# Optimization experiments

Hardware: AMD Instinct MI355X
Metric: run time of the kernel (lower is better)

## Reference

```python
import jax, jax.numpy as jnp
import numpy as np

# Faithful distillation of AttentionNet's cross-modal attention block.
# The resnet50/PointNet backbones are replaced by their output feature maps
# (img: [B,256,64,64], pc2d: [B,2048,64,64]) supplied as inputs, since the
# kernel-relevant math is the conv1x1 projections + bmm/softmax/bmm attention,
# followed by global avg-pool, concat, and the fc + log_softmax head.
# Note: the original forward contains a bug (img_v1 overwritten by img.view)
# and dead code; we implement the clearly intended attention math.

B, CQ, CK, H, W = 16, 256, 2048, 64, 64
NUM_CLASS = 40


def conv1x1(x, w, b):
    # x: [B,Cin,H,W], w: [Cout,Cin], b: [Cout]
    return jnp.einsum('bchw,oc->bohw', x, w) + b[None, :, None, None]


def setup_inputs() -> dict:
    key = jax.random.key(0)
    ks = jax.random.split(key, 16)
    s = lambda fan_in: 1.0 / np.sqrt(fan_in)
    return {
        'img': jax.random.normal(ks[0], (B, CQ, H, W), jnp.float32),
        'pc2d': jax.random.normal(ks[1], (B, CK, H, W), jnp.float32),
        'Wq': jax.random.normal(ks[2], (CQ, CQ), jnp.float32) * s(CQ),
        'bq': jnp.zeros((CQ,), jnp.float32),
        'Wk': jax.random.normal(ks[3], (CQ, CK), jnp.float32) * s(CK),
        'bk': jnp.zeros((CQ,), jnp.float32),
        'Wvi': jax.random.normal(ks[4], (CQ, CQ), jnp.float32) * s(CQ),
        'bvi': jnp.zeros((CQ,), jnp.float32),
        'Wvp': jax.random.normal(ks[5], (CK, CK), jnp.float32) * s(CK),
        'bvp': jnp.zeros((CK,), jnp.float32),
        'gamma1': jnp.zeros((1,), jnp.float32),
        'W1': jax.random.normal(ks[6], (1024, CQ + CK), jnp.float32) * s(CQ + CK),
        'b1': jnp.zeros((1024,), jnp.float32),
        'W2': jax.random.normal(ks[7], (NUM_CLASS, 1024), jnp.float32) * s(1024),
        'b2': jnp.zeros((NUM_CLASS,), jnp.float32),
    }


def reference(img, pc2d, Wq, bq, Wk, bk, Wvi, bvi, Wvp, bvp, gamma1, W1, b1, W2, b2):
    N = H * W  # 4096
    q = conv1x1(img, Wq, bq).reshape(B, CQ, N).transpose(0, 2, 1)   # [B,N,256]
    k = conv1x1(pc2d, Wk, bk).reshape(B, CQ, N)                     # [B,256,N]
    att = jax.nn.softmax(jnp.einsum('bnc,bcm->bnm', q, k), axis=-1)  # [B,N,N]
    # image branch: out = gamma * bmm(V_img, att^T) + img
    vi = conv1x1(img, Wvi, bvi).reshape(B, CQ, N)
    img_att = jnp.einsum('bcn,bmn->bcm', vi, att).reshape(B, CQ, H, W)
    img_out = gamma1[0] * img_att + img
    # point-cloud branch: bmm(V_pc, att^T)
    vp = conv1x1(pc2d, Wvp, bvp).reshape(B, CK, N)
    pc_out = jnp.einsum('bcn,bmn->bcm', vp, att)                    # [B,2048,N]
    # global average pool + concat + MLP head with log_softmax
    img_feat = img_out.mean(axis=(2, 3))                            # [B,256]
    pc_feat = pc_out.mean(axis=2)                                   # [B,2048]
    fused = jnp.concatenate([img_feat, pc_feat], axis=-1)           # [B,2304]
    h = jax.nn.relu(fused @ W1.T + b1)
    logits = h @ W2.T + b2
    return jax.nn.log_softmax(logits, axis=1)
```

## Files before the change

### kernel.cpp

```cpp
#include <hip/hip_runtime.h>
#include <cstdint>

typedef __attribute__((ext_vector_type(8))) short short8;
typedef __attribute__((ext_vector_type(4))) float f32x4;

#define LOG2E 1.44269504088896340736f
#define SHIFT 64.0f

__device__ __forceinline__ unsigned short f2bf(float x) {
  union { float f; unsigned u; } c; c.f = x;
  unsigned r = c.u + 0x7fffu + ((c.u >> 16) & 1u);
  return (unsigned short)(r >> 16);
}

__device__ __forceinline__ void gl2lds16(const void* g, void* l) {
  __builtin_amdgcn_global_load_lds((const __attribute__((address_space(1))) void*)g,
                                   (__attribute__((address_space(3))) void*)l, 16, 0, 0);
}

__global__ void cvt_bf16(const float* __restrict__ src, unsigned short* __restrict__ dst, int n4) {
  int i = blockIdx.x * 256 + threadIdx.x;
  if (i >= n4) return;
  float4 v = ((const float4*)src)[i];
  ushort4 o;
  o.x = f2bf(v.x); o.y = f2bf(v.y); o.z = f2bf(v.z); o.w = f2bf(v.w);
  ((ushort4*)dst)[i] = o;
}

__device__ __forceinline__ void stage_tile_async(unsigned short* lds, const unsigned short* src,
                                                 int w, int lane) {
  const int r8 = lane >> 3;
  const int gx = (lane & 7) ^ r8;
  const char* gbase = (const char*)src + (size_t)(w * 32 + r8) * 512 + gx * 16;
  char* lbase = (char*)lds + (w * 32) * 128;
#pragma unroll
  for (int p = 0; p < 4; ++p)
    gl2lds16(gbase + (size_t)p * 8 * 512, lbase + p * 1024);
}

__device__ __forceinline__ void mfma_step(const unsigned short* A, const unsigned short* B,
                                          int aBase, int bBase, const int poff0, const int poff1,
                                          f32x4 acc[4][4]) {
#pragma unroll
  for (int ks = 0; ks < 2; ++ks) {
    const int po = ks ? poff1 : poff0;
    short8 af[4], bfr[4];
#pragma unroll
    for (int mt = 0; mt < 4; ++mt) af[mt] = *(const short8*)&A[aBase + mt * 1024 + po];
#pragma unroll
    for (int nt = 0; nt < 4; ++nt) bfr[nt] = *(const short8*)&B[bBase + nt * 1024 + po];
#pragma unroll
    for (int mt = 0; mt < 4; ++mt)
#pragma unroll
      for (int nt = 0; nt < 4; ++nt)
        acc[mt][nt] = __builtin_amdgcn_mfma_f32_16x16x32_bf16(af[mt], bfr[nt], acc[mt][nt], 0, 0, 0);
  }
}

__global__ __launch_bounds__(256, 2) void attn_rowsum(
    const unsigned short* __restrict__ qt, const unsigned short* __restrict__ kt,
    float* __restrict__ row_l) {
  __shared__ unsigned short Ab[2][128 * 64];
  __shared__ unsigned short Bb[2][128 * 64];
  __shared__ float lred[2][128];
  const int b = blockIdx.y, i0 = blockIdx.x * 128;
  const int t = threadIdx.x, w = t >> 6, lane = t & 63, q = lane >> 4, ln = lane & 15;
  const int ihalf = w >> 1, jhalf = w & 1;
  const unsigned short* qbase = qt + ((size_t)b * 4096 + i0) * 256;
  const unsigned short* kbase = kt + (size_t)b * 4096 * 256;
  const int poff0 = ((q) ^ (ln & 7)) * 8;
  const int poff1 = ((4 + q) ^ (ln & 7)) * 8;
  const int aBase = (ihalf * 64 + ln) * 64;
  const int bBase = (jhalf * 64 + ln) * 64;
  float lacc[4][4] = {};

  stage_tile_async(Ab[0], qbase, w, lane);
  stage_tile_async(Bb[0], kbase, w, lane);
  __syncthreads();

  for (int jt = 0; jt < 32; ++jt) {
    f32x4 acc[4][4] = {};
#pragma unroll 1
    for (int ch = 0; ch < 4; ++ch) {
      const int s = jt * 4 + ch;
      if (s + 1 < 128) {
        const int jn = (s + 1) >> 2, cn = (s + 1) & 3;
        stage_tile_async(Ab[(s + 1) & 1], qbase + cn * 64, w, lane);
        stage_tile_async(Bb[(s + 1) & 1], kbase + (size_t)jn * 128 * 256 + cn * 64, w, lane);
      }
      mfma_step(Ab[s & 1], Bb[s & 1], aBase, bBase, poff0, poff1, acc);
      __syncthreads();
    }
#pragma unroll
    for (int mt = 0; mt < 4; ++mt)
#pragma unroll
      for (int r = 0; r < 4; ++r) {
        float e = exp2f(acc[mt][0][r] * LOG2E - SHIFT) + exp2f(acc[mt][1][r] * LOG2E - SHIFT)
                + exp2f(acc[mt][2][r] * LOG2E - SHIFT) + exp2f(acc[mt][3][r] * LOG2E - SHIFT);
        e += __shfl_xor(e, 1); e += __shfl_xor(e, 2);
        e += __shfl_xor(e, 4); e += __shfl_xor(e, 8);
        lacc[mt][r] += e;
      }
  }
  if (ln == 0) {
#pragma unroll
    for (int mt = 0; mt < 4; ++mt)
#pragma unroll
      for (int r = 0; r < 4; ++r)
        lred[jhalf][ihalf * 64 + mt * 16 + q * 4 + r] = lacc[mt][r];
  }
  __syncthreads();
  if (t < 128) row_l[b * 4096 + i0 + t] = lred[0][t] + lred[1][t];
}

__global__ void inv_kernel(const float* __restrict__ l, float* __restrict__ linv) {
  int i = blockIdx.x * 256 + threadIdx.x;
  linv[i] = 1.0f / l[i];
}

__global__ __launch_bounds__(256, 2) void attn_colsum(
    const unsigned short* __restrict__ qt, const unsigned short* __restrict__ kt,
    const float* __restrict__ linv, float* __restrict__ s_col) {
  __shared__ unsigned short Ab[2][128 * 64];
  __shared__ unsigned short Bb[2][128 * 64];
  __shared__ float sred[2][128];
  const int b = blockIdx.y, j0 = blockIdx.x * 128;
  const int t = threadIdx.x, w = t >> 6, lane = t & 63, q = lane >> 4, ln = lane & 15;
  const int ihalf = w >> 1, jhalf = w & 1;
  const unsigned short* qbase = qt + (size_t)b * 4096 * 256;
  const unsigned short* kb = kt + ((size_t)b * 4096 + j0) * 256;
  const int poff0 = ((q) ^ (ln & 7)) * 8;
  const int poff1 = ((4 + q) ^ (ln & 7)) * 8;
  const int aBase = (ihalf * 64 + ln) * 64;
  const int bBase = (jhalf * 64 + ln) * 64;
  float scacc[4] = {};

  stage_tile_async(Ab[0], qbase, w, lane);
  stage_tile_async(Bb[0], kb, w, lane);
  __syncthreads();

  for (int it = 0; it < 32; ++it) {
    const float4* lp = (const float4*)(linv + (size_t)b * 4096 + it * 128 + ihalf * 64 + q * 4);
    float4 lv[4];
#pragma unroll
    for (int mt = 0; mt < 4; ++mt) lv[mt] = lp[mt * 4];

    f32x4 acc[4][4] = {};
#pragma unroll 1
    for (int ch = 0; ch < 4; ++ch) {
      const int s = it * 4 + ch;
      if (s + 1 < 128) {
        const int in_ = (s + 1) >> 2, cn = (s + 1) & 3;
        stage_tile_async(Ab[(s + 1) & 1], qbase + (size_t)in_ * 128 * 256 + cn * 64, w, lane);
        stage_tile_async(Bb[(s + 1) & 1], kb + cn * 64, w, lane);
      }
      mfma_step(Ab[s & 1], Bb[s & 1], aBase, bBase, poff0, poff1, acc);
      __syncthreads();
    }
#pragma unroll
    for (int nt = 0; nt < 4; ++nt) {
      float v = 0.f;
#pragma unroll
      for (int mt = 0; mt < 4; ++mt) {
        v += exp2f(acc[mt][nt][0] * LOG2E - SHIFT) * lv[mt].x;
        v += exp2f(acc[mt][nt][1] * LOG2E - SHIFT) * lv[mt].y;
        v += exp2f(acc[mt][nt][2] * LOG2E - SHIFT) * lv[mt].z;
        v += exp2f(acc[mt][nt][3] * LOG2E - SHIFT) * lv[mt].w;
      }
      v += __shfl_xor(v, 16); v += __shfl_xor(v, 32);
      scacc[nt] += v;
    }
  }
  if (q == 0) {
#pragma unroll
    for (int nt = 0; nt < 4; ++nt)
      sred[ihalf][jhalf * 64 + nt * 16 + ln] = scacc[nt];
  }
  __syncthreads();
  if (t < 128) s_col[b * 4096 + j0 + t] = sred[0][t] + sred[1][t];
}

__global__ __launch_bounds__(256, 2) void proj_kernel(
    const float* __restrict__ In, const unsigned short* __restrict__ Wbf,
    const float* __restrict__ bias, unsigned short* __restrict__ Out, int Kdim) {
  __shared__ unsigned short Alds[64 * 72];
  __shared__ unsigned short Blds[256 * 72];
  const int b = blockIdx.y, sp0 = blockIdx.x * 64;
  const int t = threadIdx.x, w = t >> 6, lane = t & 63, q = lane >> 4, ln = lane & 15;
  f32x4 acc[4][4] = {};
  const int nch = Kdim >> 6;
  for (int ch = 0; ch < nch; ++ch) {
    const int ci0 = ch * 64;
#pragma unroll
    for (int p = 0; p < 8; ++p) {
      int s = t + 256 * p;
      int row = s >> 3, sl = s & 7;
      *(uint4*)(&Blds[row * 72 + sl * 8]) = *(const uint4*)(&Wbf[(size_t)row * Kdim + ci0 + sl * 8]);
    }
    {
      const int cp = t >> 3, spg = t & 7;
      const float* r0 = In + ((size_t)b * Kdim + ci0 + 2 * cp) * 4096 + sp0 + spg * 8;
      const float* r1 = r0 + 4096;
      float4 a0 = *(const float4*)(r0);
      float4 a1 = *(const float4*)(r0 + 4);
      float4 b0 = *(const float4*)(r1);
      float4 b1 = *(const float4*)(r1 + 4);
      float va[8] = {a0.x, a0.y, a0.z, a0.w, a1.x, a1.y, a1.z, a1.w};
      float vb[8] = {b0.x, b0.y, b0.z, b0.w, b1.x, b1.y, b1.z, b1.w};
#pragma unroll
      for (int k2 = 0; k2 < 8; ++k2) {
        unsigned u0 = f2bf(va[k2]), u1 = f2bf(vb[k2]);
        *(unsigned*)(&Alds[(spg * 8 + k2) * 72 + 2 * cp]) = u0 | (u1 << 16);
      }
    }
    __syncthreads();
#pragma unroll
    for (int ks = 0; ks < 2; ++ks) {
      short8 af[4], bfr[4];
#pragma unroll
      for (int mt = 0; mt < 4; ++mt)
        af[mt] = *(const short8*)(&Alds[(mt * 16 + ln) * 72 + ks * 32 + q * 8]);
#pragma unroll
      for (int nt = 0; nt < 4; ++nt)
        bfr[nt] = *(const short8*)(&Blds[(w * 64 + nt * 16 + ln) * 72 + ks * 32 + q * 8]);
#pragma unroll
      for (int mt = 0; mt < 4; ++mt)
#pragma unroll
        for (int nt = 0; nt < 4; ++nt)
          acc[mt][nt] = __builtin_amdgcn_mfma_f32_16x16x32_bf16(af[mt], bfr[nt], acc[mt][nt], 0, 0, 0);
    }
    __syncthreads();
  }
#pragma unroll
  for (int nt = 0; nt < 4; ++nt) {
    int co = w * 64 + nt * 16 + ln;
    float bv = bias[co];
#pragma unroll
    for (int mt = 0; mt < 4; ++mt)
#pragma unroll
      for (int r = 0; r < 4; ++r) {
        int sp = sp0 + mt * 16 + q * 4 + r;
        Out[((size_t)b * 4096 + sp) * 256 + co] = f2bf(acc[mt][nt][r] + bv);
      }
  }
}

__global__ void sbar_kernel(const float* __restrict__ s_col, float* __restrict__ sbar) {
  const int b = blockIdx.x, t = threadIdx.x;
  float v = 0.f;
  for (int k = 0; k < 16; ++k) v += s_col[b * 4096 + t + 256 * k];
  for (int m = 1; m < 64; m <<= 1) v += __shfl_xor(v, m);
  __shared__ float red[4];
  if ((t & 63) == 0) red[t >> 6] = v;
  __syncthreads();
  if (t == 0) sbar[b] = (red[0] + red[1] + red[2] + red[3]) * (1.f / 4096.f);
}

__global__ void pool_kernel(const float* __restrict__ img, const float* __restrict__ pc2d,
                            const float* __restrict__ s_col, float* __restrict__ u_pool,
                            float* __restrict__ imean, float* __restrict__ t_pool) {
  const int b = blockIdx.y, chunk = blockIdx.x;
  const int t = threadIdx.x, ch_l = t >> 2, j = t & 3;
  const bool isimg = chunk < 4;
  int ch;
  const float4* row4;
  if (isimg) {
    ch = chunk * 64 + ch_l;
    row4 = (const float4*)(img + ((size_t)b * 256 + ch) * 4096);
  } else {
    ch = (chunk - 4) * 64 + ch_l;
    row4 = (const float4*)(pc2d + ((size_t)b * 2048 + ch) * 4096);
  }
  const float4* s4 = (const float4*)(s_col + b * 4096);
  float accd = 0.f, accs = 0.f;
  for (int kk = 0; kk < 256; ++kk) {
    float4 x = row4[j + 4 * kk];
    float4 sv = s4[j + 4 * kk];
    accd += x.x * sv.x + x.y * sv.y + x.z * sv.z + x.w * sv.w;
    accs += x.x + x.y + x.z + x.w;
  }
  accd += __shfl_xor(accd, 1); accd += __shfl_xor(accd, 2);
  accs += __shfl_xor(accs, 1); accs += __shfl_xor(accs, 2);
  if (j == 0) {
    if (isimg) {
      u_pool[b * 256 + ch] = accd * (1.f / 4096.f);
      imean[b * 256 + ch] = accs * (1.f / 4096.f);
    } else {
      t_pool[b * 2048 + ch] = accd * (1.f / 4096.f);
    }
  }
}

__global__ void imgfeat_kernel(const float* __restrict__ Wvi, const float* __restrict__ bvi,
                               const float* __restrict__ gamma1, const float* __restrict__ u_pool,
                               const float* __restrict__ imean, const float* __restrict__ sbar,
                               float* __restrict__ fused) {
  const int t = threadIdx.x;
  const int co = blockIdx.x * 64 + (t >> 2), j = t & 3;
  float acc[16];
#pragma unroll
  for (int b = 0; b < 16; ++b) acc[b] = 0.f;
  const float4* w4 = (const float4*)(Wvi + (size_t)co * 256);
  for (int kk = 0; kk < 16; ++kk) {
    float4 wv = w4[j + 4 * kk];
#pragma unroll
    for (int b = 0; b < 16; ++b) {
      float4 uv = ((const float4*)(u_pool + b * 256))[j + 4 * kk];
      acc[b] += wv.x * uv.x + wv.y * uv.y + wv.z * uv.z + wv.w * uv.w;
    }
  }
#pragma unroll
  for (int b = 0; b < 16; ++b) { acc[b] += __shfl_xor(acc[b], 1); acc[b] += __shfl_xor(acc[b], 2); }
  if (j == 0) {
    float g = gamma1[0], bv = bvi[co];
#pragma unroll
    for (int b = 0; b < 16; ++b)
      fused[b * 2304 + co] = g * (acc[b] + bv * sbar[b]) + imean[b * 256 + co];
  }
}

__global__ void pcfeat_kernel(const float* __restrict__ Wvp, const float* __restrict__ bvp,
                              const float* __restrict__ t_pool, const float* __restrict__ sbar,
                              float* __restrict__ fused) {
  const int t = threadIdx.x;
  const int co = blockIdx.x * 64 + (t >> 2), j = t & 3;
  float acc[16];
#pragma unroll
  for (int b = 0; b < 16; ++b) acc[b] = 0.f;
  const float4* w4 = (const float4*)(Wvp + (size_t)co * 2048);
  for (int kk = 0; kk < 128; ++kk) {
    float4 wv = w4[j + 4 * kk];
#pragma unroll
    for (int b = 0; b < 16; ++b) {
      float4 tv = ((const float4*)(t_pool + b * 2048))[j + 4 * kk];
      acc[b] += wv.x * tv.x + wv.y * tv.y + wv.z * tv.z + wv.w * tv.w;
    }
  }
#pragma unroll
  for (int b = 0; b < 16; ++b) { acc[b] += __shfl_xor(acc[b], 1); acc[b] += __shfl_xor(acc[b], 2); }
  if (j == 0) {
    float bv = bvp[co];
#pragma unroll
    for (int b = 0; b < 16; ++b)
      fused[b * 2304 + 256 + co] = acc[b] + bv * sbar[b];
  }
}

__global__ void head1_kernel(const float* __restrict__ W1, const float* __restrict__ b1,
                             const float* __restrict__ fused, float* __restrict__ h) {
  const int t = threadIdx.x;
  const int o = blockIdx.x * 64 + (t >> 2), j = t & 3;
  float acc[16];
#pragma unroll
  for (int b = 0; b < 16; ++b) acc[b] = 0.f;
  const float4* w4 = (const float4*)(W1 + (size_t)o * 2304);
  for (int kk = 0; kk < 144; ++kk) {
    float4 wv = w4[j + 4 * kk];
#pragma unroll
    for (int b = 0; b < 16; ++b) {
      float4 fv = ((const float4*)(fused + b * 2304))[j + 4 * kk];
      acc[b] += wv.x * fv.x + wv.y * fv.y + wv.z * fv.z + wv.w * fv.w;
    }
  }
#pragma unroll
  for (int b = 0; b < 16; ++b) { acc[b] += __shfl_xor(acc[b], 1); acc[b] += __shfl_xor(acc[b], 2); }
  if (j == 0) {
    float bv = b1[o];
#pragma unroll
    for (int b = 0; b < 16; ++b) h[b * 1024 + o] = fmaxf(acc[b] + bv, 0.f);
  }
}

__global__ void head2_kernel(const float* __restrict__ W2, const float* __restrict__ b2,
                             const float* __restrict__ h, float* __restrict__ out) {
  const int b = blockIdx.x, t = threadIdx.x;
  __shared__ float logit[40];
  __shared__ float red[4];
  float4 hv = ((const float4*)(h + b * 1024))[t];
  for (int c = 0; c < 40; ++c) {
    float4 wv = ((const float4*)(W2 + (size_t)c * 1024))[t];
    float p = wv.x * hv.x + wv.y * hv.y + wv.z * hv.z + wv.w * hv.w;
    for (int m = 1; m < 64; m <<= 1) p += __shfl_xor(p, m);
    if ((t & 63) == 0) red[t >> 6] = p;
    __syncthreads();
    if (t == 0) logit[c] = red[0] + red[1] + red[2] + red[3] + b2[c];
    __syncthreads();
  }
  if (t == 0) {
    float mx = -1e30f;
    for (int c = 0; c < 40; ++c) mx = fmaxf(mx, logit[c]);
    float s = 0.f;
    for (int c = 0; c < 40; ++c) s += expf(logit[c] - mx);
    float ls = logf(s);
    for (int c = 0; c < 40; ++c) out[b * 40 + c] = logit[c] - mx - ls;
  }
}

extern "C" void kernel_launch(void* const* d_in, const int* in_sizes, int n_in,
                              void* d_out, int out_size, void* d_ws, size_t ws_size,
                              hipStream_t stream) {
  (void)in_sizes; (void)n_in; (void)out_size; (void)ws_size;
  const float* img    = (const float*)d_in[0];
  const float* pc2d   = (const float*)d_in[1];
  const float* Wq     = (const float*)d_in[2];
  const float* bq     = (const float*)d_in[3];
  const float* Wk     = (const float*)d_in[4];
  const float* bk     = (const float*)d_in[5];
  const float* Wvi    = (const float*)d_in[6];
  const float* bvi    = (const float*)d_in[7];
  const float* Wvp    = (const float*)d_in[8];
  const float* bvp    = (const float*)d_in[9];
  const float* gamma1 = (const float*)d_in[10];
  const float* W1     = (const float*)d_in[11];
  const float* b1     = (const float*)d_in[12];
  const float* W2     = (const float*)d_in[13];
  const float* b2     = (const float*)d_in[14];

  char* ws = (char*)d_ws;
  unsigned short* q_t   = (unsigned short*)(ws + 0);
  unsigned short* k_t   = (unsigned short*)(ws + 33554432);
  unsigned short* wq_bf = (unsigned short*)(ws + 67108864);
  unsigned short* wk_bf = (unsigned short*)(ws + 67239936);
  float* linv   = (float*)(ws + 68288512);
  float* row_l  = (float*)(ws + 68550656);
  float* s_col  = (float*)(ws + 68812800);
  float* sbar   = (float*)(ws + 69074944);
  float* u_pool = (float*)(ws + 69075008);
  float* imean  = (float*)(ws + 69091392);
  float* t_pool = (float*)(ws + 69107776);
  float* fusedb = (float*)(ws + 69238848);
  float* h_buf  = (float*)(ws + 69386304);

  cvt_bf16<<<dim3(64), dim3(256), 0, stream>>>(Wq, wq_bf, 16384);
  cvt_bf16<<<dim3(512), dim3(256), 0, stream>>>(Wk, wk_bf, 131072);

  proj_kernel<<<dim3(64, 16), dim3(256), 0, stream>>>(img, wq_bf, bq, q_t, 256);
  proj_kernel<<<dim3(64, 16), dim3(256), 0, stream>>>(pc2d, wk_bf, bk, k_t, 2048);

  attn_rowsum<<<dim3(32, 16), dim3(256), 0, stream>>>(q_t, k_t, row_l);
  inv_kernel<<<dim3(256), dim3(256), 0, stream>>>(row_l, linv);
  attn_colsum<<<dim3(32, 16), dim3(256), 0, stream>>>(q_t, k_t, linv, s_col);

  sbar_kernel<<<dim3(16), dim3(256), 0, stream>>>(s_col, sbar);
  pool_kernel<<<dim3(36, 16), dim3(256), 0, stream>>>(img, pc2d, s_col, u_pool, imean, t_pool);

  imgfeat_kernel<<<dim3(4), dim3(256), 0, stream>>>(Wvi, bvi, gamma1, u_pool, imean, sbar, fusedb);
  pcfeat_kernel<<<dim3(32), dim3(256), 0, stream>>>(Wvp, bvp, t_pool, sbar, fusedb);

  head1_kernel<<<dim3(16), dim3(256), 0, stream>>>(W1, b1, fusedb, h_buf);
  head2_kernel<<<dim3(16), dim3(256), 0, stream>>>(W2, b2, h_buf, (float*)d_out);
}
```

Baseline: 1.722 ms.

## Keep full 128x256 resident tile in LDS and stream only the other operand

The row-sum and col-sum attention kernels now load the fixed operand tile (Q rows or K rows, full 256-deep channel dimension) once into 64KB of dynamic LDS, and double-buffer only the streamed operand in 32-channel chunks. This removes the repeated global reloads of the fixed tile on every j/i iteration, halving per-step global traffic. In exchange it uses 80KB of LDS per block, which may lower occupancy below the two blocks per CU the launch bounds target, and it doubles the number of barriers per tile.

```diff
diff --git a/kernel.cpp b/kernel.cpp
--- a/kernel.cpp
+++ b/kernel.cpp
@@ -27,68 +27,67 @@
   ((ushort4*)dst)[i] = o;
 }
 
-__device__ __forceinline__ void stage_tile_async(unsigned short* lds, const unsigned short* src,
-                                                 int w, int lane) {
-  const int r8 = lane >> 3;
-  const int gx = (lane & 7) ^ r8;
-  const char* gbase = (const char*)src + (size_t)(w * 32 + r8) * 512 + gx * 16;
-  char* lbase = (char*)lds + (w * 32) * 128;
-#pragma unroll
-  for (int p = 0; p < 4; ++p)
-    gl2lds16(gbase + (size_t)p * 8 * 512, lbase + p * 1024);
-}
-
-__device__ __forceinline__ void mfma_step(const unsigned short* A, const unsigned short* B,
-                                          int aBase, int bBase, const int poff0, const int poff1,
-                                          f32x4 acc[4][4]) {
-#pragma unroll
-  for (int ks = 0; ks < 2; ++ks) {
-    const int po = ks ? poff1 : poff0;
-    short8 af[4], bfr[4];
-#pragma unroll
-    for (int mt = 0; mt < 4; ++mt) af[mt] = *(const short8*)&A[aBase + mt * 1024 + po];
-#pragma unroll
-    for (int nt = 0; nt < 4; ++nt) bfr[nt] = *(const short8*)&B[bBase + nt * 1024 + po];
-#pragma unroll
-    for (int mt = 0; mt < 4; ++mt)
-#pragma unroll
-      for (int nt = 0; nt < 4; ++nt)
-        acc[mt][nt] = __builtin_amdgcn_mfma_f32_16x16x32_bf16(af[mt], bfr[nt], acc[mt][nt], 0, 0, 0);
-  }
+__device__ __forceinline__ void stage_resident(char* ldsbase, const char* src, int w, int lane) {
+  const int p = lane & 31;
+  const int rlo = lane >> 5;
+#pragma unroll
+  for (int it = 0; it < 16; ++it) {
+    const int r = w * 32 + it * 2 + rlo;
+    const int gs = (p & 24) | ((p & 7) ^ (r & 7));
+    gl2lds16(src + (size_t)r * 512 + gs * 16, ldsbase + (w * 16 + it) * 1024);
+  }
+}
+
+__device__ __forceinline__ void stage_stream(char* buf, const char* srcbase, int roff0, int roff1,
+                                             int w) {
+  gl2lds16(srcbase + roff0, buf + w * 1024);
+  gl2lds16(srcbase + roff1, buf + 4096 + w * 1024);
 }
 
 __global__ __launch_bounds__(256, 2) void attn_rowsum(
     const unsigned short* __restrict__ qt, const unsigned short* __restrict__ kt,
     float* __restrict__ row_l) {
-  __shared__ unsigned short Ab[2][128 * 64];
-  __shared__ unsigned short Bb[2][128 * 64];
-  __shared__ float lred[2][128];
+  extern __shared__ char pool[];
   const int b = blockIdx.y, i0 = blockIdx.x * 128;
   const int t = threadIdx.x, w = t >> 6, lane = t & 63, q = lane >> 4, ln = lane & 15;
   const int ihalf = w >> 1, jhalf = w & 1;
-  const unsigned short* qbase = qt + ((size_t)b * 4096 + i0) * 256;
-  const unsigned short* kbase = kt + (size_t)b * 4096 * 256;
-  const int poff0 = ((q) ^ (ln & 7)) * 8;
-  const int poff1 = ((4 + q) ^ (ln & 7)) * 8;
-  const int aBase = (ihalf * 64 + ln) * 64;
-  const int bBase = (jhalf * 64 + ln) * 64;
+  const char* qres = (const char*)(qt + ((size_t)b * 4096 + i0) * 256);
+  const char* kb = (const char*)(kt + (size_t)b * 4096 * 256);
+  const int rr0 = w * 16 + (lane >> 2);
+  const int gsS = (lane & 3) ^ ((lane >> 3) & 3);
+  const int roff0 = rr0 * 512 + gsS * 16;
+  const int roff1 = (64 + rr0) * 512 + gsS * 16;
+  const int aRow = (ihalf * 64 + ln) * 512;
+  const int bRow = jhalf * 4096 + ln * 64 + (q ^ ((ln >> 1) & 3)) * 16;
   float lacc[4][4] = {};
 
-  stage_tile_async(Ab[0], qbase, w, lane);
-  stage_tile_async(Bb[0], kbase, w, lane);
+  stage_resident(pool, qres, w, lane);
+  stage_stream(pool + 65536, kb, roff0, roff1, w);
   __syncthreads();
 
+#pragma unroll 1
   for (int jt = 0; jt < 32; ++jt) {
     f32x4 acc[4][4] = {};
-#pragma unroll 1
-    for (int ch = 0; ch < 4; ++ch) {
-      const int s = jt * 4 + ch;
-      if (s + 1 < 128) {
-        const int jn = (s + 1) >> 2, cn = (s + 1) & 3;
-        stage_tile_async(Ab[(s + 1) & 1], qbase + cn * 64, w, lane);
-        stage_tile_async(Bb[(s + 1) & 1], kbase + (size_t)jn * 128 * 256 + cn * 64, w, lane);
-      }
-      mfma_step(Ab[s & 1], Bb[s & 1], aBase, bBase, poff0, poff1, acc);
+#pragma unroll
+    for (int c = 0; c < 8; ++c) {
+      const int s = jt * 8 + c;
+      if (s + 1 < 256) {
+        const int njt = (s + 1) >> 3, nc = (s + 1) & 7;
+        stage_stream(pool + 65536 + ((s + 1) & 1) * 8192,
+                     kb + (size_t)njt * 65536 + nc * 64, roff0, roff1, w);
+      }
+      const char* B = pool + 65536 + (s & 1) * 8192;
+      const int posA = ((4 * c) & 24) | ((4 * (c & 1) + q) ^ (ln & 7));
+      short8 af[4], bfr[4];
+#pragma unroll
+      for (int mt = 0; mt < 4; ++mt) af[mt] = *(const short8*)(pool + aRow + mt * 8192 + posA * 16);
+#pragma unroll
+      for (int nt = 0; nt < 4; ++nt) bfr[nt] = *(const short8*)(B + bRow + nt * 1024);
+#pragma unroll
+      for (int mt = 0; mt < 4; ++mt)
+#pragma unroll
+        for (int nt = 0; nt < 4; ++nt)
+          acc[mt][nt] = __builtin_amdgcn_mfma_f32_16x16x32_bf16(af[mt], bfr[nt], acc[mt][nt], 0, 0, 0);
       __syncthreads();
     }
 #pragma unroll
@@ -102,15 +101,16 @@
         lacc[mt][r] += e;
       }
   }
+  float* lred = (float*)(pool + 65536);
   if (ln == 0) {
 #pragma unroll
     for (int mt = 0; mt < 4; ++mt)
 #pragma unroll
       for (int r = 0; r < 4; ++r)
-        lred[jhalf][ihalf * 64 + mt * 16 + q * 4 + r] = lacc[mt][r];
+        lred[jhalf * 128 + ihalf * 64 + mt * 16 + q * 4 + r] = lacc[mt][r];
   }
   __syncthreads();
-  if (t < 128) row_l[b * 4096 + i0 + t] = lred[0][t] + lred[1][t];
+  if (t < 128) row_l[b * 4096 + i0 + t] = lred[t] + lred[128 + t];
 }
 
 __global__ void inv_kernel(const float* __restrict__ l, float* __restrict__ linv) {
@@ -121,24 +121,25 @@
 __global__ __launch_bounds__(256, 2) void attn_colsum(
     const unsigned short* __restrict__ qt, const unsigned short* __restrict__ kt,
     const float* __restrict__ linv, float* __restrict__ s_col) {
-  __shared__ unsigned short Ab[2][128 * 64];
-  __shared__ unsigned short Bb[2][128 * 64];
-  __shared__ float sred[2][128];
+  extern __shared__ char pool[];
   const int b = blockIdx.y, j0 = blockIdx.x * 128;
   const int t = threadIdx.x, w = t >> 6, lane = t & 63, q = lane >> 4, ln = lane & 15;
   const int ihalf = w >> 1, jhalf = w & 1;
-  const unsigned short* qbase = qt + (size_t)b * 4096 * 256;
-  const unsigned short* kb = kt + ((size_t)b * 4096 + j0) * 256;
-  const int poff0 = ((q) ^ (ln & 7)) * 8;
-  const int poff1 = ((4 + q) ^ (ln & 7)) * 8;
-  const int aBase = (ihalf * 64 + ln) * 64;
-  const int bBase = (jhalf * 64 + ln) * 64;
+  const char* kres = (const char*)(kt + ((size_t)b * 4096 + j0) * 256);
+  const char* qb = (const char*)(qt + (size_t)b * 4096 * 256);
+  const int rr0 = w * 16 + (lane >> 2);
+  const int gsS = (lane & 3) ^ ((lane >> 3) & 3);
+  const int roff0 = rr0 * 512 + gsS * 16;
+  const int roff1 = (64 + rr0) * 512 + gsS * 16;
+  const int aRow = ihalf * 4096 + ln * 64 + (q ^ ((ln >> 1) & 3)) * 16;
+  const int bRow = (jhalf * 64 + ln) * 512;
   float scacc[4] = {};
 
-  stage_tile_async(Ab[0], qbase, w, lane);
-  stage_tile_async(Bb[0], kb, w, lane);
+  stage_resident(pool, kres, w, lane);
+  stage_stream(pool + 65536, qb, roff0, roff1, w);
   __syncthreads();
 
+#pragma unroll 1
   for (int it = 0; it < 32; ++it) {
     const float4* lp = (const float4*)(linv + (size_t)b * 4096 + it * 128 + ihalf * 64 + q * 4);
     float4 lv[4];
@@ -146,15 +147,26 @@
     for (int mt = 0; mt < 4; ++mt) lv[mt] = lp[mt * 4];
 
     f32x4 acc[4][4] = {};
-#pragma unroll 1
-    for (int ch = 0; ch < 4; ++ch) {
-      const int s = it * 4 + ch;
-      if (s + 1 < 128) {
-        const int in_ = (s + 1) >> 2, cn = (s + 1) & 3;
-        stage_tile_async(Ab[(s + 1) & 1], qbase + (size_t)in_ * 128 * 256 + cn * 64, w, lane);
-        stage_tile_async(Bb[(s + 1) & 1], kb + cn * 64, w, lane);
-      }
-      mfma_step(Ab[s & 1], Bb[s & 1], aBase, bBase, poff0, poff1, acc);
+#pragma unroll
+    for (int c = 0; c < 8; ++c) {
+      const int s = it * 8 + c;
+      if (s + 1 < 256) {
+        const int nit = (s + 1) >> 3, nc = (s + 1) & 7;
+        stage_stream(pool + 65536 + ((s + 1) & 1) * 8192,
+                     qb + (size_t)nit * 65536 + nc * 64, roff0, roff1, w);
+      }
+      const char* A = pool + 65536 + (s & 1) * 8192;
+      const int posB = ((4 * c) & 24) | ((4 * (c & 1) + q) ^ (ln & 7));
+      short8 af[4], bfr[4];
+#pragma unroll
+      for (int mt = 0; mt < 4; ++mt) af[mt] = *(const short8*)(A + aRow + mt * 1024);
+#pragma unroll
+      for (int nt = 0; nt < 4; ++nt) bfr[nt] = *(const short8*)(pool + bRow + nt * 8192 + posB * 16);
+#pragma unroll
+      for (int mt = 0; mt < 4; ++mt)
+#pragma unroll
+        for (int nt = 0; nt < 4; ++nt)
+          acc[mt][nt] = __builtin_amdgcn_mfma_f32_16x16x32_bf16(af[mt], bfr[nt], acc[mt][nt], 0, 0, 0);
       __syncthreads();
     }
 #pragma unroll
@@ -171,13 +183,14 @@
       scacc[nt] += v;
     }
   }
+  float* sred = (float*)(pool + 65536);
   if (q == 0) {
 #pragma unroll
     for (int nt = 0; nt < 4; ++nt)
-      sred[ihalf][jhalf * 64 + nt * 16 + ln] = scacc[nt];
+      sred[ihalf * 128 + jhalf * 64 + nt * 16 + ln] = scacc[nt];
   }
   __syncthreads();
-  if (t < 128) s_col[b * 4096 + j0 + t] = sred[0][t] + sred[1][t];
+  if (t < 128) s_col[b * 4096 + j0 + t] = sred[t] + sred[128 + t];
 }
 
 __global__ __launch_bounds__(256, 2) void proj_kernel(
@@ -431,15 +444,18 @@
   float* fusedb = (float*)(ws + 69238848);
   float* h_buf  = (float*)(ws + 69386304);
 
+  hipFuncSetAttribute((const void*)attn_rowsum, hipFuncAttributeMaxDynamicSharedMemorySize, 81920);
+  hipFuncSetAttribute((const void*)attn_colsum, hipFuncAttributeMaxDynamicSharedMemorySize, 81920);
+
   cvt_bf16<<<dim3(64), dim3(256), 0, stream>>>(Wq, wq_bf, 16384);
   cvt_bf16<<<dim3(512), dim3(256), 0, stream>>>(Wk, wk_bf, 131072);
 
   proj_kernel<<<dim3(64, 16), dim3(256), 0, stream>>>(img, wq_bf, bq, q_t, 256);
   proj_kernel<<<dim3(64, 16), dim3(256), 0, stream>>>(pc2d, wk_bf, bk, k_t, 2048);
 
-  attn_rowsum<<<dim3(32, 16), dim3(256), 0, stream>>>(q_t, k_t, row_l);
+  attn_rowsum<<<dim3(32, 16), dim3(256), 81920, stream>>>(q_t, k_t, row_l);
   inv_kernel<<<dim3(256), dim3(256), 0, stream>>>(row_l, linv);
-  attn_colsum<<<dim3(32, 16), dim3(256), 0, stream>>>(q_t, k_t, linv, s_col);
+  attn_colsum<<<dim3(32, 16), dim3(256), 81920, stream>>>(q_t, k_t, linv, s_col);
 
   sbar_kernel<<<dim3(16), dim3(256), 0, stream>>>(s_col, sbar);
   pool_kernel<<<dim3(36, 16), dim3(256), 0, stream>>>(img, pc2d, s_col, u_pool, imean, t_pool);
```

Measured after the change: 1.650 ms. 4.1% less time.
